# Kernel tuning notes

Measured on AMD Instinct MI355X. Metric: run time of the kernel, lower is better.

Reference implementation:

```python
import jax, jax.numpy as jnp
import numpy as np

B = 16384; NF = 16; VOCAB = 100000; ED = 32; NNUM = 13
E = 8; T = 2; H0 = 512; H1 = 256; TH = 128
D0 = NF * ED + NNUM  # 525
EPS = 1e-5


def setup_inputs() -> dict:
    key = jax.random.key(0)
    ks = jax.random.split(key, 24)
    f32 = jnp.float32
    return {
        "categorical_x": jax.random.randint(ks[0], (B, NF), 0, VOCAB),
        "numerical_x": jax.random.normal(ks[1], (B, NNUM), f32),
        "epoch": 5,  # >= M -> MoE (not if_neuron) branch
        "emb_table": jax.random.normal(ks[2], (NF * VOCAB, ED), f32) * 0.05,
        "W0": jax.random.normal(ks[3], (E, D0, H0), f32) * 0.05,
        "b0": jnp.zeros((E, H0), f32),
        "bn0_gamma": 1.0 + 0.1 * jax.random.normal(ks[4], (H0,), f32),
        "bn0_beta": 0.1 * jax.random.normal(ks[5], (H0,), f32),
        "bn0_mean": 0.1 * jax.random.normal(ks[6], (H0,), f32),
        "bn0_var": 0.5 + jax.random.uniform(ks[7], (H0,), f32),
        "W1": jax.random.normal(ks[8], (E, H0, H1), f32) * 0.05,
        "b1": jnp.zeros((E, H1), f32),
        "bn1_gamma": 1.0 + 0.1 * jax.random.normal(ks[9], (H1,), f32),
        "bn1_beta": 0.1 * jax.random.normal(ks[10], (H1,), f32),
        "bn1_mean": 0.1 * jax.random.normal(ks[11], (H1,), f32),
        "bn1_var": 0.5 + jax.random.uniform(ks[12], (H1,), f32),
        "Wg": jax.random.normal(ks[13], (T, D0, E), f32) * 0.05,
        "bg": jnp.zeros((T, E), f32),
        "Wt1": jax.random.normal(ks[14], (T, H1, TH), f32) * 0.05,
        "bt1": jnp.zeros((T, TH), f32),
        "tbn_gamma": 1.0 + 0.1 * jax.random.normal(ks[15], (T, TH), f32),
        "tbn_beta": 0.1 * jax.random.normal(ks[16], (T, TH), f32),
        "tbn_mean": 0.1 * jax.random.normal(ks[17], (T, TH), f32),
        "tbn_var": 0.5 + jax.random.uniform(ks[18], (T, TH), f32),
        "Wt2": jax.random.normal(ks[19], (T, TH, 1), f32) * 0.05,
        "bt2": jnp.zeros((T, 1), f32),
    }


def reference(categorical_x, numerical_x, epoch, emb_table,
              W0, b0, bn0_gamma, bn0_beta, bn0_mean, bn0_var,
              W1, b1, bn1_gamma, bn1_beta, bn1_mean, bn1_var,
              Wg, bg, Wt1, bt1, tbn_gamma, tbn_beta, tbn_mean, tbn_var,
              Wt2, bt2):
    # --- embedding + concat ---
    offsets = jnp.arange(NF, dtype=categorical_x.dtype) * VOCAB
    emb = emb_table[categorical_x + offsets[None, :]].reshape(B, NF * ED)
    x = jnp.concatenate([emb, numerical_x], axis=1)  # [B, D0]

    def bn(h, g, b, m, v):  # eval-mode BatchNorm1d, params shared across experts
        return (h - m) * jax.lax.rsqrt(v + EPS) * g + b

    # --- per-expert layer 0: grouped GEMM + shared BN/ReLU (Dropout eval=id) ---
    h = jnp.einsum('bd,edk->ebk', x, W0) + b0[:, None, :]          # [E,B,H0]
    h = jax.nn.relu(bn(h, bn0_gamma, bn0_beta, bn0_mean, bn0_var))
    # --- per-expert layer 1 ---
    h = jnp.einsum('ebd,edk->ebk', h, W1) + b1[:, None, :]          # [E,B,H1]
    h = jax.nn.relu(bn(h, bn1_gamma, bn1_beta, bn1_mean, bn1_var))

    expert_output = jnp.transpose(h, (1, 0, 2))                     # [B,E,H1]
    # --- per-task softmax gates over the raw input, bmm combine ---
    gates = jax.nn.softmax(jnp.einsum('bd,tde->tbe', x, Wg) + bg[:, None, :], axis=-1)  # [T,B,E]
    fea = jnp.einsum('tbe,bek->tbk', gates, expert_output)          # [T,B,H1]

    # --- per-task tower MLP: Linear -> BN -> ReLU -> Linear, sigmoid ---
    t = jnp.einsum('tbk,tkh->tbh', fea, Wt1) + bt1[:, None, :]      # [T,B,TH]
    t = (t - tbn_mean[:, None, :]) * jax.lax.rsqrt(tbn_var[:, None, :] + EPS)
    t = jax.nn.relu(t * tbn_gamma[:, None, :] + tbn_beta[:, None, :])
    out = (jnp.einsum('tbh,tho->tbo', t, Wt2) + bt2[:, None, :])[..., 0]  # [T,B]
    return jax.nn.sigmoid(out)
```

## Files before the change

### kernel.cpp

```cpp
#include <hip/hip_runtime.h>
#include <hip/hip_bf16.h>

#define B_ 16384
#define NF_ 16
#define VOCAB_ 100000
#define ED_ 32
#define NNUM_ 13
#define E_ 8
#define T_ 2
#define H0_ 512
#define H1_ 256
#define TH_ 128
#define D0_ 525
#define K0P 640

typedef __bf16 bf16x8 __attribute__((ext_vector_type(8)));
typedef float  f32x4  __attribute__((ext_vector_type(4)));

typedef __attribute__((address_space(3))) void lds_void;
typedef __attribute__((address_space(1))) const void gbl_void;

__device__ __forceinline__ void load_lds16f(const void* g, void* l) {
  __builtin_amdgcn_global_load_lds((gbl_void*)g, (lds_void*)l, 16, 0, 0);
}

#define BARX                                        \
  do {                                              \
    asm volatile("" ::: "memory");                  \
    __builtin_amdgcn_s_barrier();                   \
    __builtin_amdgcn_sched_barrier(0);              \
    asm volatile("" ::: "memory");                  \
  } while (0)
#define LGKM0                                       \
  do {                                              \
    asm volatile("s_waitcnt lgkmcnt(0)" ::: "memory"); \
    __builtin_amdgcn_sched_barrier(0);              \
  } while (0)

__global__ __launch_bounds__(256) void k_embed(const int* __restrict__ cat,
                                               const float* __restrict__ num,
                                               const float* __restrict__ emb,
                                               __hip_bfloat16* __restrict__ x) {
  int b = blockIdx.x;
  int t = threadIdx.x;
  const int* crow = cat + b * NF_;
#pragma unroll
  for (int i = 0; i < 3; ++i) {
    int d = t + i * 256;
    if (d >= K0P) continue;
    float v;
    if (d < 512) {
      int f = d >> 5, c = d & 31;
      v = emb[((long long)(f * VOCAB_ + crow[f])) * ED_ + c];
    } else if (d < D0_) {
      v = num[b * NNUM_ + (d - 512)];
    } else {
      v = 0.f;
    }
    x[(long long)b * K0P + d] = __float2bfloat16(v);
  }
}

__global__ __launch_bounds__(256) void k_wprep(const float* __restrict__ W,
                                               __hip_bfloat16* __restrict__ Wp,
                                               int K, int N, int KP) {
  __shared__ float tile[64][65];
  int k0 = blockIdx.x * 64, n0 = blockIdx.y * 64, e = blockIdx.z;
  int tx = threadIdx.x & 63, ty = threadIdx.x >> 6;
  for (int r = ty; r < 64; r += 4) {
    int k = k0 + r;
    tile[r][tx] = (k < K) ? W[((long long)e * K + k) * N + n0 + tx] : 0.f;
  }
  __syncthreads();
  for (int r = ty; r < 64; r += 4) {
    int n = n0 + r;
    Wp[((long long)e * N + n) * KP + k0 + tx] = __float2bfloat16(tile[tx][r]);
  }
}

__global__ void k_prep_small(const float* b0, const float* g0, const float* be0,
                             const float* m0, const float* v0,
                             const float* b1, const float* g1, const float* be1,
                             const float* m1, const float* v1,
                             const float* bt1, const float* tg, const float* tb,
                             const float* tm, const float* tv,
                             float* scale0, float* ebias0, float* scale1, float* ebias1,
                             float* tscale, float* tbias) {
  int i = blockIdx.x * 256 + threadIdx.x;
  if (i < H0_) scale0[i] = g0[i] * rsqrtf(v0[i] + 1e-5f);
  if (i < H1_) scale1[i] = g1[i] * rsqrtf(v1[i] + 1e-5f);
  if (i < T_ * TH_) {
    float s = tg[i] * rsqrtf(tv[i] + 1e-5f);
    tscale[i] = s;
    tbias[i] = (bt1[i] - tm[i]) * s + tb[i];
  }
  if (i < E_ * H0_) {
    int n = i & (H0_ - 1);
    float s = g0[n] * rsqrtf(v0[n] + 1e-5f);
    ebias0[i] = (b0[i] - m0[n]) * s + be0[n];
  }
  if (i < E_ * H1_) {
    int n = i & (H1_ - 1);
    float s = g1[n] * rsqrtf(v1[n] + 1e-5f);
    ebias1[i] = (b1[i] - m1[n]) * s + be1[n];
  }
}

__global__ __launch_bounds__(256) void k_gates(const __hip_bfloat16* __restrict__ x,
                                               const float* __restrict__ Wg,
                                               const float* __restrict__ bg,
                                               float* __restrict__ gates) {
  int gidx = blockIdx.x * 256 + threadIdx.x;
  int b = gidx >> 4, te = gidx & 15;
  int t = te >> 3, e = te & 7;
  const __hip_bfloat16* xr = x + (long long)b * K0P;
  const float* wg = Wg + ((long long)t * D0_) * E_ + e;
  float acc = bg[t * E_ + e];
  int k = 0;
  for (; k + 8 <= D0_; k += 8) {
    bf16x8 xv = *reinterpret_cast<const bf16x8*>(xr + k);
#pragma unroll
    for (int j = 0; j < 8; ++j)
      acc += (float)xv[j] * wg[(long long)(k + j) * E_];
  }
  for (; k < D0_; ++k) acc += __bfloat162float(xr[k]) * wg[(long long)k * E_];
  float mx = acc;
#pragma unroll
  for (int o = 1; o < 8; o <<= 1) mx = fmaxf(mx, __shfl_xor(mx, o));
  float p = __expf(acc - mx);
  float s = p;
#pragma unroll
  for (int o = 1; o < 8; o <<= 1) s += __shfl_xor(s, o);
  gates[((long long)t * B_ + b) * E_ + e] = p / s;
}

__global__ __launch_bounds__(512, 2) void k_gemm(
    const __hip_bfloat16* __restrict__ Aall, long long strideAe, int lda,
    const __hip_bfloat16* __restrict__ Ball, long long strideBe, int ldb,
    __hip_bfloat16* __restrict__ Call, long long strideCe, int N,
    const float* __restrict__ scale, const float* __restrict__ ebias, int strideEb,
    int K) {
  __shared__ __align__(16) char As[2][2][16384];
  __shared__ __align__(16) char Bs[2][2][16384];

  const int e = blockIdx.z;
  const char* A = reinterpret_cast<const char*>(Aall + (long long)e * strideAe +
                                                (long long)blockIdx.x * 256 * lda);
  const char* Bw = reinterpret_cast<const char*>(Ball + (long long)e * strideBe +
                                                 (long long)blockIdx.y * 256 * ldb);
  const int ldab = lda * 2, ldbb = ldb * 2;

  const int tid = threadIdx.x;
  const int lane = tid & 63;
  const int wid = tid >> 6;
  const int wq_r = wid >> 2, wq_c = wid & 3;

  const int srow = tid >> 3;
  const int swz = ((tid & 7) << 4) ^ ((srow & 7) << 4);

  auto STG_A = [&](int kt, int half, int slot) {
#pragma unroll
    for (int j = 0; j < 2; ++j) {
      const int lrow = srow + j * 64;
      load_lds16f(A + (long long)(half * 128 + lrow) * ldab + kt * 128 + swz,
                  &As[slot][half][j * 8192 + tid * 16]);
    }
  };
  auto STG_B = [&](int kt, int half, int slot) {
#pragma unroll
    for (int j = 0; j < 2; ++j) {
      const int lrow = srow + j * 64;
      load_lds16f(Bw + (long long)(half * 128 + lrow) * ldbb + kt * 128 + swz,
                  &Bs[slot][half][j * 8192 + tid * 16]);
    }
  };

  bf16x8 af[2][4], bq[2][2];
  auto LDA = [&](int slot, int half) {
#pragma unroll
    for (int kk = 0; kk < 2; ++kk) {
      const int kb = kk * 64 + (lane >> 4) * 16;
#pragma unroll
      for (int m = 0; m < 4; ++m) {
        const int lrow = wq_r * 64 + m * 16 + (lane & 15);
        af[kk][m] = *reinterpret_cast<const bf16x8*>(
            &As[slot][half][lrow * 128 + (kb ^ ((lane & 7) << 4))]);
      }
    }
  };
  auto LDB = [&](int slot, int half) {
#pragma unroll
    for (int kk = 0; kk < 2; ++kk) {
      const int kb = kk * 64 + (lane >> 4) * 16;
#pragma unroll
      for (int n = 0; n < 2; ++n) {
        const int lrow = wq_c * 32 + n * 16 + (lane & 15);
        bq[kk][n] = *reinterpret_cast<const bf16x8*>(
            &Bs[slot][half][lrow * 128 + (kb ^ ((lane & 7) << 4))]);
      }
    }
  };

  f32x4 acc[2][2][4][2];
#pragma unroll
  for (int a = 0; a < 2; ++a)
#pragma unroll
    for (int b = 0; b < 2; ++b)
#pragma unroll
      for (int m = 0; m < 4; ++m)
#pragma unroll
        for (int n = 0; n < 2; ++n) acc[a][b][m][n] = (f32x4){0.f, 0.f, 0.f, 0.f};

#define MMQ(QM, QN)                                                            \
  do {                                                                         \
    __builtin_amdgcn_s_setprio(1);                                             \
    _Pragma("unroll") for (int kk = 0; kk < 2; ++kk)                           \
        _Pragma("unroll") for (int m = 0; m < 4; ++m)                          \
            _Pragma("unroll") for (int n = 0; n < 2; ++n)                      \
                acc[QM][QN][m][n] = __builtin_amdgcn_mfma_f32_16x16x32_bf16(   \
                    af[kk][m], bq[kk][n], acc[QM][QN][m][n], 0, 0, 0);         \
    __builtin_amdgcn_s_setprio(0);                                             \
  } while (0)

  const int nk = K / 64;
  const int nj = nk / 2;

  STG_A(0, 0, 0); STG_A(0, 1, 0); STG_B(0, 0, 0); STG_B(0, 1, 0);
  if (nk > 1) { STG_A(1, 0, 1); STG_B(1, 1, 1); }
  asm volatile("s_waitcnt vmcnt(4)" ::: "memory");
  BARX;

  for (int j = 0; j < nj; ++j) {
    const int t1 = 2 * j + 1, t2 = 2 * j + 2, t3 = 2 * j + 3;
    const bool more = (t2 < nk);
    LDA(0, 0); LDB(0, 0);
    STG_A(t1, 1, 1);
    BARX; LGKM0; MMQ(0, 0); BARX;
    LDB(0, 1);
    STG_B(t1, 0, 1);
    BARX; LGKM0; MMQ(0, 1); BARX;
    LDA(0, 1);
    if (more) STG_A(t2, 0, 0);
    BARX; LGKM0; MMQ(1, 1); BARX;
    LDB(0, 0);
    if (more) STG_B(t2, 1, 0);
    BARX; LGKM0; MMQ(1, 0);
    if (more) { asm volatile("s_waitcnt vmcnt(4)" ::: "memory"); }
    else      { asm volatile("s_waitcnt vmcnt(0)" ::: "memory"); }
    BARX;
    LDA(1, 0); LDB(1, 0);
    if (more) STG_A(t2, 1, 0);
    BARX; LGKM0; MMQ(0, 0); BARX;
    LDB(1, 1);
    if (more) STG_B(t2, 0, 0);
    BARX; LGKM0; MMQ(0, 1); BARX;
    LDA(1, 1);
    if (more) STG_A(t3, 0, 1);
    BARX; LGKM0; MMQ(1, 1); BARX;
    LDB(1, 0);
    if (more) STG_B(t3, 1, 1);
    BARX; LGKM0; MMQ(1, 0);
    if (more) { asm volatile("s_waitcnt vmcnt(4)" ::: "memory"); }
    BARX;
  }
#undef MMQ

  __hip_bfloat16* C = Call + (long long)e * strideCe;
  const float* eb = ebias + e * strideEb;
  const int m0 = blockIdx.x * 256, n0 = blockIdx.y * 256;
#pragma unroll
  for (int Qm = 0; Qm < 2; ++Qm)
#pragma unroll
    for (int Qn = 0; Qn < 2; ++Qn)
#pragma unroll
      for (int n = 0; n < 2; ++n) {
        const int col = n0 + Qn * 128 + wq_c * 32 + n * 16 + (lane & 15);
        const float s = scale[col];
        const float bb = eb[col];
#pragma unroll
        for (int m = 0; m < 4; ++m) {
          const int rowb = m0 + Qm * 128 + wq_r * 64 + m * 16 + (lane >> 4) * 4;
#pragma unroll
          for (int i = 0; i < 4; ++i) {
            float v = fmaxf(acc[Qm][Qn][m][n][i] * s + bb, 0.f);
            C[(long long)(rowb + i) * N + col] = __float2bfloat16(v);
          }
        }
      }
}

__global__ __launch_bounds__(256) void k_combine(const __hip_bfloat16* __restrict__ h1,
                                                 const float* __restrict__ gates,
                                                 __hip_bfloat16* __restrict__ fea) {
  const int idx = blockIdx.x * 256 + threadIdx.x;
  const int b = idx >> 5, c = idx & 31;
  const f32x4* gp0 = reinterpret_cast<const f32x4*>(gates + (long long)b * E_);
  const f32x4* gp1 = reinterpret_cast<const f32x4*>(gates + ((long long)B_ + b) * E_);
  const f32x4 g0lo = gp0[0], g0hi = gp0[1];
  const f32x4 g1lo = gp1[0], g1hi = gp1[1];

  float a0[8], a1[8];
#pragma unroll
  for (int j = 0; j < 8; ++j) { a0[j] = 0.f; a1[j] = 0.f; }

#pragma unroll
  for (int ee = 0; ee < 8; ++ee) {
    bf16x8 hv = *reinterpret_cast<const bf16x8*>(
        h1 + ((long long)ee * B_ + b) * H1_ + c * 8);
    const float ga = (ee < 4) ? g0lo[ee & 3] : g0hi[ee & 3];
    const float gb = (ee < 4) ? g1lo[ee & 3] : g1hi[ee & 3];
#pragma unroll
    for (int j = 0; j < 8; ++j) {
      float v = (float)hv[j];
      a0[j] += ga * v;
      a1[j] += gb * v;
    }
  }
  bf16x8 o0, o1;
#pragma unroll
  for (int j = 0; j < 8; ++j) { o0[j] = (__bf16)a0[j]; o1[j] = (__bf16)a1[j]; }
  *reinterpret_cast<bf16x8*>(fea + (long long)b * H1_ + c * 8) = o0;
  *reinterpret_cast<bf16x8*>(fea + ((long long)B_ + b) * H1_ + c * 8) = o1;
}

__global__ __launch_bounds__(256) void k_tower2(
    const __hip_bfloat16* __restrict__ fea, const float* __restrict__ Wt1,
    const float* __restrict__ Wt2, const float* __restrict__ bt2,
    const float* __restrict__ tscale, const float* __restrict__ tbias,
    float* __restrict__ out) {
  __shared__ __align__(16) char Ws[TH_ * 512];
  const int t = blockIdx.y;
  const int tid = threadIdx.x;
  const int lane = tid & 63, wv = tid >> 6;

  const int row = blockIdx.x * 64 + wv * 16 + (lane & 15);
  const int g4 = lane >> 4;

  for (int it = 0; it < 16; ++it) {
    int idx = it * 256 + tid;
    int h = idx & 127, kc = idx >> 7;
    bf16x8 v;
#pragma unroll
    for (int j = 0; j < 8; ++j)
      v[j] = (__bf16)Wt1[((long long)t * H1_ + kc * 8 + j) * TH_ + h];
    int byt = h * 512 + ((kc * 16) ^ ((h & 7) << 4));
    *reinterpret_cast<bf16x8*>(Ws + byt) = v;
  }

  bf16x8 af[8];
  {
    const __hip_bfloat16* fp = fea + ((long long)t * B_ + row) * H1_ + g4 * 8;
#pragma unroll
    for (int c = 0; c < 8; ++c)
      af[c] = *reinterpret_cast<const bf16x8*>(fp + c * 32);
  }
  __syncthreads();

  f32x4 acc[8];
#pragma unroll
  for (int n = 0; n < 8; ++n) acc[n] = (f32x4){0.f, 0.f, 0.f, 0.f};
#pragma unroll
  for (int c = 0; c < 8; ++c) {
    int kb = c * 64 + g4 * 16;
#pragma unroll
    for (int n = 0; n < 8; ++n) {
      int hrow = n * 16 + (lane & 15);
      bf16x8 bv = *reinterpret_cast<const bf16x8*>(Ws + hrow * 512 + (kb ^ ((hrow & 7) << 4)));
      acc[n] = __builtin_amdgcn_mfma_f32_16x16x32_bf16(af[c], bv, acc[n], 0, 0, 0);
    }
  }

  float part[4] = {0.f, 0.f, 0.f, 0.f};
#pragma unroll
  for (int n = 0; n < 8; ++n) {
    int col = n * 16 + (lane & 15);
    float s = tscale[t * TH_ + col], bb = tbias[t * TH_ + col], w2 = Wt2[t * TH_ + col];
#pragma unroll
    for (int i = 0; i < 4; ++i)
      part[i] += fmaxf(acc[n][i] * s + bb, 0.f) * w2;
  }
#pragma unroll
  for (int o = 1; o < 16; o <<= 1) {
#pragma unroll
    for (int i = 0; i < 4; ++i) part[i] += __shfl_xor(part[i], o);
  }
  if ((lane & 15) == 0) {
    int rbase = blockIdx.x * 64 + wv * 16 + g4 * 4;
    float b2 = bt2[t];
#pragma unroll
    for (int i = 0; i < 4; ++i) {
      float z = part[i] + b2;
      out[(long long)t * B_ + rbase + i] = 1.f / (1.f + __expf(-z));
    }
  }
}

extern "C" void kernel_launch(void* const* d_in, const int* in_sizes, int n_in,
                              void* d_out, int out_size, void* d_ws, size_t ws_size,
                              hipStream_t stream) {
  const int*   cat = (const int*)d_in[0];
  const float* num = (const float*)d_in[1];
  const float* emb = (const float*)d_in[3];
  const float* W0  = (const float*)d_in[4];
  const float* b0  = (const float*)d_in[5];
  const float* g0  = (const float*)d_in[6];
  const float* be0 = (const float*)d_in[7];
  const float* m0  = (const float*)d_in[8];
  const float* v0  = (const float*)d_in[9];
  const float* W1  = (const float*)d_in[10];
  const float* b1  = (const float*)d_in[11];
  const float* g1  = (const float*)d_in[12];
  const float* be1 = (const float*)d_in[13];
  const float* m1  = (const float*)d_in[14];
  const float* v1  = (const float*)d_in[15];
  const float* Wg  = (const float*)d_in[16];
  const float* bg  = (const float*)d_in[17];
  const float* Wt1 = (const float*)d_in[18];
  const float* bt1 = (const float*)d_in[19];
  const float* tg  = (const float*)d_in[20];
  const float* tb  = (const float*)d_in[21];
  const float* tm  = (const float*)d_in[22];
  const float* tv  = (const float*)d_in[23];
  const float* Wt2 = (const float*)d_in[24];
  const float* bt2 = (const float*)d_in[25];
  float* out = (float*)d_out;

  char* ws = (char*)d_ws;
  if (ws_size < 247496704ULL) return;

  __hip_bfloat16* x_bf = (__hip_bfloat16*)(ws + 0ULL);
  __hip_bfloat16* W0p  = (__hip_bfloat16*)(ws + 20971520ULL);
  __hip_bfloat16* W1p  = (__hip_bfloat16*)(ws + 26214400ULL);
  float* gates   = (float*)(ws + 28311552ULL);
  float* scale0  = (float*)(ws + 29360128ULL);
  float* ebias0  = (float*)(ws + 29362176ULL);
  float* scale1  = (float*)(ws + 29378560ULL);
  float* ebias1  = (float*)(ws + 29379584ULL);
  float* tscale  = (float*)(ws + 29387776ULL);
  float* tbias   = (float*)(ws + 29388800ULL);
  __hip_bfloat16* h0  = (__hip_bfloat16*)(ws + 29392896ULL);
  __hip_bfloat16* h1  = (__hip_bfloat16*)(ws + 163610624ULL);
  __hip_bfloat16* fea = (__hip_bfloat16*)(ws + 230719488ULL);

  k_wprep<<<dim3(K0P / 64, H0_ / 64, E_), 256, 0, stream>>>(W0, W0p, D0_, H0_, K0P);
  k_wprep<<<dim3(H0_ / 64, H1_ / 64, E_), 256, 0, stream>>>(W1, W1p, H0_, H1_, H0_);
  k_prep_small<<<16, 256, 0, stream>>>(b0, g0, be0, m0, v0, b1, g1, be1, m1, v1,
                                       bt1, tg, tb, tm, tv,
                                       scale0, ebias0, scale1, ebias1, tscale, tbias);
  k_embed<<<B_, 256, 0, stream>>>(cat, num, emb, x_bf);
  k_gates<<<B_ * 16 / 256, 256, 0, stream>>>(x_bf, Wg, bg, gates);
  k_gemm<<<dim3(B_ / 256, H0_ / 256, E_), 512, 0, stream>>>(
      x_bf, 0LL, K0P, W0p, (long long)H0_ * K0P, K0P,
      h0, (long long)B_ * H0_, H0_, scale0, ebias0, H0_, K0P);
  k_gemm<<<dim3(B_ / 256, H1_ / 256, E_), 512, 0, stream>>>(
      h0, (long long)B_ * H0_, H0_, W1p, (long long)H1_ * H0_, H0_,
      h1, (long long)B_ * H1_, H1_, scale1, ebias1, H1_, H0_);
  k_combine<<<B_ * H1_ / 8 / 256, 256, 0, stream>>>(h1, gates, fea);
  k_tower2<<<dim3(B_ / 64, T_), 256, 0, stream>>>(fea, Wt1, Wt2, bt2,
                                                  tscale, tbias, out);
}
```

Baseline: 257.6 us.

## Trim layer-0 K padding and stage GEMM epilogue through LDS for coalesced stores

Reduces the padded K of the first expert GEMM from 640 to 576, which gives an odd number of 64-wide K tiles. To support that, the main loop gets a separate guard for the third prefetch and a tail step that handles the final odd tile. The epilogue now writes bf16 results into swizzled shared memory (reusing the staging buffers) and then stores 16-byte rows to global memory, replacing scattered 2-byte stores. This removes wasted MFMA work on padding and uncoalesced output writes, at the cost of an extra barrier and a shared-memory round trip.

```diff
diff --git a/kernel.cpp b/kernel.cpp
--- a/kernel.cpp
+++ b/kernel.cpp
@@ -12,7 +12,7 @@
 #define H1_ 256
 #define TH_ 128
 #define D0_ 525
-#define K0P 640
+#define K0P 576
 
 typedef __bf16 bf16x8 __attribute__((ext_vector_type(8)));
 typedef float  f32x4  __attribute__((ext_vector_type(4)));
@@ -140,8 +140,9 @@
     __hip_bfloat16* __restrict__ Call, long long strideCe, int N,
     const float* __restrict__ scale, const float* __restrict__ ebias, int strideEb,
     int K) {
-  __shared__ __align__(16) char As[2][2][16384];
-  __shared__ __align__(16) char Bs[2][2][16384];
+  __shared__ __align__(16) char SMEM[131072];
+  char (*As)[2][16384] = reinterpret_cast<char (*)[2][16384]>(SMEM);
+  char (*Bs)[2][16384] = reinterpret_cast<char (*)[2][16384]>(SMEM + 65536);
 
   const int e = blockIdx.z;
   const char* A = reinterpret_cast<const char*>(Aall + (long long)e * strideAe +
@@ -223,7 +224,7 @@
   } while (0)
 
   const int nk = K / 64;
-  const int nj = nk / 2;
+  const int nj = nk >> 1;
 
   STG_A(0, 0, 0); STG_A(0, 1, 0); STG_B(0, 0, 0); STG_B(0, 1, 0);
   if (nk > 1) { STG_A(1, 0, 1); STG_B(1, 1, 1); }
@@ -233,6 +234,7 @@
   for (int j = 0; j < nj; ++j) {
     const int t1 = 2 * j + 1, t2 = 2 * j + 2, t3 = 2 * j + 3;
     const bool more = (t2 < nk);
+    const bool more3 = (t3 < nk);
     LDA(0, 0); LDB(0, 0);
     STG_A(t1, 1, 1);
     BARX; LGKM0; MMQ(0, 0); BARX;
@@ -255,16 +257,26 @@
     if (more) STG_B(t2, 0, 0);
     BARX; LGKM0; MMQ(0, 1); BARX;
     LDA(1, 1);
-    if (more) STG_A(t3, 0, 1);
+    if (more3) STG_A(t3, 0, 1);
     BARX; LGKM0; MMQ(1, 1); BARX;
     LDB(1, 0);
-    if (more) STG_B(t3, 1, 1);
+    if (more3) STG_B(t3, 1, 1);
     BARX; LGKM0; MMQ(1, 0);
     if (more) { asm volatile("s_waitcnt vmcnt(4)" ::: "memory"); }
     BARX;
   }
+
+  if (nk & 1) {
+    asm volatile("s_waitcnt vmcnt(0)" ::: "memory");
+    BARX;
+    LDA(0, 0); LDB(0, 0); LGKM0; MMQ(0, 0);
+    LDB(0, 1);            LGKM0; MMQ(0, 1);
+    LDA(0, 1);            LGKM0; MMQ(1, 1);
+    LDB(0, 0);            LGKM0; MMQ(1, 0);
+  }
 #undef MMQ
 
+  __syncthreads();
   __hip_bfloat16* C = Call + (long long)e * strideCe;
   const float* eb = ebias + e * strideEb;
   const int m0 = blockIdx.x * 256, n0 = blockIdx.y * 256;
@@ -274,19 +286,30 @@
     for (int Qn = 0; Qn < 2; ++Qn)
 #pragma unroll
       for (int n = 0; n < 2; ++n) {
-        const int col = n0 + Qn * 128 + wq_c * 32 + n * 16 + (lane & 15);
-        const float s = scale[col];
-        const float bb = eb[col];
+        const int col = Qn * 128 + wq_c * 32 + n * 16 + (lane & 15);
+        const float s = scale[n0 + col];
+        const float bb = eb[n0 + col];
 #pragma unroll
         for (int m = 0; m < 4; ++m) {
-          const int rowb = m0 + Qm * 128 + wq_r * 64 + m * 16 + (lane >> 4) * 4;
 #pragma unroll
           for (int i = 0; i < 4; ++i) {
-            float v = fmaxf(acc[Qm][Qn][m][n][i] * s + bb, 0.f);
-            C[(long long)(rowb + i) * N + col] = __float2bfloat16(v);
+            const int row = Qm * 128 + wq_r * 64 + m * 16 + (lane >> 4) * 4 + i;
+            const float v = fmaxf(acc[Qm][Qn][m][n][i] * s + bb, 0.f);
+            const int byt = row * 512 + ((((col >> 3) ^ (row & 7)) << 4) | ((col & 7) << 1));
+            *reinterpret_cast<__hip_bfloat16*>(SMEM + byt) = __float2bfloat16(v);
           }
         }
       }
+  __syncthreads();
+#pragma unroll
+  for (int it = 0; it < 16; ++it) {
+    const int row = it * 16 + (tid >> 5);
+    const int c16 = tid & 31;
+    const f32x4 d = *reinterpret_cast<const f32x4*>(
+        SMEM + row * 512 + ((c16 ^ (row & 7)) << 4));
+    *reinterpret_cast<f32x4*>(
+        reinterpret_cast<char*>(C + (long long)(m0 + row) * N + n0) + c16 * 16) = d;
+  }
 }
 
 __global__ __launch_bounds__(256) void k_combine(const __hip_bfloat16* __restrict__ h1,
```

After: 402.8 us. 1.56x slower.

## Make grouped GEMMs persistent with cross-tile prefetch and LDS-staged coalesced epilogue

Applied to the files above, without the earlier changes.

Replaces the per-tile GEMM grid with a persistent kernel of 256 blocks. Each block walks several consecutive output tiles (4 for layer 0, 2 for layer 1), and the k-loop pipeline runs continuously across tile boundaries, so the next tile's loads overlap the current tile's tail. The epilogue now writes through a swizzled LDS buffer so global stores are 16-byte coalesced instead of scattered 2-byte writes, and tile order is remapped across blocks. The costs are one block per CU (launch bounds drop from 2 to 1), a 160KB LDS footprint, and extra barriers inside the epilogue.

```diff
diff --git a/kernel.cpp b/kernel.cpp
--- a/kernel.cpp
+++ b/kernel.cpp
@@ -134,21 +134,22 @@
   gates[((long long)t * B_ + b) * E_ + e] = p / s;
 }
 
-__global__ __launch_bounds__(512, 2) void k_gemm(
-    const __hip_bfloat16* __restrict__ Aall, long long strideAe, int lda,
-    const __hip_bfloat16* __restrict__ Ball, long long strideBe, int ldb,
-    __hip_bfloat16* __restrict__ Call, long long strideCe, int N,
-    const float* __restrict__ scale, const float* __restrict__ ebias, int strideEb,
-    int K) {
-  __shared__ __align__(16) char As[2][2][16384];
-  __shared__ __align__(16) char Bs[2][2][16384];
-
-  const int e = blockIdx.z;
-  const char* A = reinterpret_cast<const char*>(Aall + (long long)e * strideAe +
-                                                (long long)blockIdx.x * 256 * lda);
-  const char* Bw = reinterpret_cast<const char*>(Ball + (long long)e * strideBe +
-                                                 (long long)blockIdx.y * 256 * ldb);
-  const int ldab = lda * 2, ldbb = ldb * 2;
+template <int KC, int NNY, int TPB>
+__global__ __launch_bounds__(512, 1) void k_gemmp(
+    const __hip_bfloat16* __restrict__ Aall, long long strideAe,
+    const __hip_bfloat16* __restrict__ Ball, long long strideBe,
+    __hip_bfloat16* __restrict__ Call, long long strideCe,
+    const float* __restrict__ scale, const float* __restrict__ ebias,
+    int strideEb) {
+  constexpr int NK = KC / 64;
+  constexpr int S = TPB * NK;
+  constexpr int P = S / 2;
+  constexpr int PPT = NK / 2;
+  constexpr int N = NNY * 256;
+  constexpr int LDAB = KC * 2;
+
+  __shared__ __align__(16) char SMEM[163840];
+  char* const Ebuf = SMEM + 131072;
 
   const int tid = threadIdx.x;
   const int lane = tid & 63;
@@ -158,25 +159,42 @@
   const int srow = tid >> 3;
   const int swz = ((tid & 7) << 4) ^ ((srow & 7) << 4);
 
-  auto STG_A = [&](int kt, int half, int slot) {
+  const int c = blockIdx.x;
+  const int vbase = ((c & 7) * 32 + (c >> 3)) * TPB;
+
+  auto decode = [&](int v, int& mx, int& ny, int& e) {
+    mx = v & 63;
+    int p = v >> 6;
+    if (NNY == 2) { ny = p & 1; e = p >> 1; }
+    else          { ny = 0;     e = p;      }
+  };
+
+  auto STG = [&](int s, int half, bool isB) {
+    const int ot = s / NK, kt = s - ot * NK;
+    int mx, ny, e;
+    decode(vbase + ot, mx, ny, e);
+    const char* base;
+    char* dst;
+    if (!isB) {
+      base = reinterpret_cast<const char*>(Aall + (long long)e * strideAe +
+                                           (long long)mx * 256 * KC);
+      dst = SMEM + (s & 1) * 32768 + half * 16384;
+    } else {
+      base = reinterpret_cast<const char*>(Ball + (long long)e * strideBe +
+                                           (long long)ny * 256 * KC);
+      dst = SMEM + 65536 + (s & 1) * 32768 + half * 16384;
+    }
 #pragma unroll
     for (int j = 0; j < 2; ++j) {
       const int lrow = srow + j * 64;
-      load_lds16f(A + (long long)(half * 128 + lrow) * ldab + kt * 128 + swz,
-                  &As[slot][half][j * 8192 + tid * 16]);
-    }
-  };
-  auto STG_B = [&](int kt, int half, int slot) {
-#pragma unroll
-    for (int j = 0; j < 2; ++j) {
-      const int lrow = srow + j * 64;
-      load_lds16f(Bw + (long long)(half * 128 + lrow) * ldbb + kt * 128 + swz,
-                  &Bs[slot][half][j * 8192 + tid * 16]);
+      load_lds16f(base + (long long)(half * 128 + lrow) * LDAB + kt * 128 + swz,
+                  dst + j * 8192 + tid * 16);
     }
   };
 
   bf16x8 af[2][4], bq[2][2];
   auto LDA = [&](int slot, int half) {
+    const char* Ab = SMEM + slot * 32768 + half * 16384;
 #pragma unroll
     for (int kk = 0; kk < 2; ++kk) {
       const int kb = kk * 64 + (lane >> 4) * 16;
@@ -184,11 +202,12 @@
       for (int m = 0; m < 4; ++m) {
         const int lrow = wq_r * 64 + m * 16 + (lane & 15);
         af[kk][m] = *reinterpret_cast<const bf16x8*>(
-            &As[slot][half][lrow * 128 + (kb ^ ((lane & 7) << 4))]);
+            Ab + lrow * 128 + (kb ^ ((lane & 7) << 4)));
       }
     }
   };
   auto LDB = [&](int slot, int half) {
+    const char* Bb = SMEM + 65536 + slot * 32768 + half * 16384;
 #pragma unroll
     for (int kk = 0; kk < 2; ++kk) {
       const int kb = kk * 64 + (lane >> 4) * 16;
@@ -196,7 +215,7 @@
       for (int n = 0; n < 2; ++n) {
         const int lrow = wq_c * 32 + n * 16 + (lane & 15);
         bq[kk][n] = *reinterpret_cast<const bf16x8*>(
-            &Bs[slot][half][lrow * 128 + (kb ^ ((lane & 7) << 4))]);
+            Bb + lrow * 128 + (kb ^ ((lane & 7) << 4)));
       }
     }
   };
@@ -222,71 +241,99 @@
     __builtin_amdgcn_s_setprio(0);                                             \
   } while (0)
 
-  const int nk = K / 64;
-  const int nj = nk / 2;
-
-  STG_A(0, 0, 0); STG_A(0, 1, 0); STG_B(0, 0, 0); STG_B(0, 1, 0);
-  if (nk > 1) { STG_A(1, 0, 1); STG_B(1, 1, 1); }
+  STG(0, 0, false); STG(0, 1, false); STG(0, 0, true); STG(0, 1, true);
+  STG(1, 0, false); STG(1, 1, true);
   asm volatile("s_waitcnt vmcnt(4)" ::: "memory");
   BARX;
 
-  for (int j = 0; j < nj; ++j) {
-    const int t1 = 2 * j + 1, t2 = 2 * j + 2, t3 = 2 * j + 3;
-    const bool more = (t2 < nk);
+  int ot_done = 0;
+#pragma unroll 1
+  for (int p = 0; p < P; ++p) {
+    const int t1 = 2 * p + 1, t2 = 2 * p + 2, t3 = 2 * p + 3;
+    const bool m2 = (t2 < S), m3 = (t3 < S);
     LDA(0, 0); LDB(0, 0);
-    STG_A(t1, 1, 1);
+    STG(t1, 1, false);
     BARX; LGKM0; MMQ(0, 0); BARX;
     LDB(0, 1);
-    STG_B(t1, 0, 1);
+    STG(t1, 0, true);
     BARX; LGKM0; MMQ(0, 1); BARX;
     LDA(0, 1);
-    if (more) STG_A(t2, 0, 0);
+    if (m2) STG(t2, 0, false);
     BARX; LGKM0; MMQ(1, 1); BARX;
     LDB(0, 0);
-    if (more) STG_B(t2, 1, 0);
+    if (m2) STG(t2, 1, true);
     BARX; LGKM0; MMQ(1, 0);
-    if (more) { asm volatile("s_waitcnt vmcnt(4)" ::: "memory"); }
-    else      { asm volatile("s_waitcnt vmcnt(0)" ::: "memory"); }
+    if (m2) { asm volatile("s_waitcnt vmcnt(4)" ::: "memory"); }
+    else    { asm volatile("s_waitcnt vmcnt(0)" ::: "memory"); }
     BARX;
     LDA(1, 0); LDB(1, 0);
-    if (more) STG_A(t2, 1, 0);
+    if (m2) STG(t2, 1, false);
     BARX; LGKM0; MMQ(0, 0); BARX;
     LDB(1, 1);
-    if (more) STG_B(t2, 0, 0);
+    if (m2) STG(t2, 0, true);
     BARX; LGKM0; MMQ(0, 1); BARX;
     LDA(1, 1);
-    if (more) STG_A(t3, 0, 1);
+    if (m3) STG(t3, 0, false);
     BARX; LGKM0; MMQ(1, 1); BARX;
     LDB(1, 0);
-    if (more) STG_B(t3, 1, 1);
+    if (m3) STG(t3, 1, true);
     BARX; LGKM0; MMQ(1, 0);
-    if (more) { asm volatile("s_waitcnt vmcnt(4)" ::: "memory"); }
+    if (m2) { asm volatile("s_waitcnt vmcnt(4)" ::: "memory"); }
     BARX;
+
+    if ((p + 1) % PPT == 0) {
+      int mx, ny, e;
+      decode(vbase + ot_done, mx, ny, e);
+      __hip_bfloat16* C = Call + (long long)e * strideCe;
+      const float* eb = ebias + e * strideEb;
+      const int m0 = mx * 256, n0 = ny * 256;
+#pragma unroll
+      for (int Qm = 0; Qm < 2; ++Qm)
+#pragma unroll
+        for (int Qn = 0; Qn < 2; ++Qn) {
+#pragma unroll
+          for (int n = 0; n < 2; ++n) {
+            const int colc = wq_c * 32 + n * 16 + (lane & 15);
+            const int gcol = n0 + Qn * 128 + colc;
+            const float s = scale[gcol];
+            const float bb = eb[gcol];
+#pragma unroll
+            for (int m = 0; m < 4; ++m) {
+#pragma unroll
+              for (int i = 0; i < 4; ++i) {
+                const int row = wq_r * 64 + m * 16 + (lane >> 4) * 4 + i;
+                const float v = fmaxf(acc[Qm][Qn][m][n][i] * s + bb, 0.f);
+                const int byt = row * 256 +
+                    ((((colc >> 3) ^ (row & 7)) << 4) | ((colc & 7) << 1));
+                *reinterpret_cast<__hip_bfloat16*>(Ebuf + byt) = __float2bfloat16(v);
+              }
+            }
+          }
+          BARX;
+#pragma unroll
+          for (int it = 0; it < 4; ++it) {
+            const int r = it * 32 + (tid >> 4);
+            const int c16 = tid & 15;
+            const f32x4 d = *reinterpret_cast<const f32x4*>(
+                Ebuf + r * 256 + ((c16 ^ (r & 7)) << 4));
+            *reinterpret_cast<f32x4*>(
+                reinterpret_cast<char*>(C + (long long)(m0 + Qm * 128 + r) * N) +
+                (n0 + Qn * 128) * 2 + c16 * 16) = d;
+          }
+          BARX;
+        }
+      ++ot_done;
+#pragma unroll
+      for (int a = 0; a < 2; ++a)
+#pragma unroll
+        for (int b = 0; b < 2; ++b)
+#pragma unroll
+          for (int m = 0; m < 4; ++m)
+#pragma unroll
+            for (int n = 0; n < 2; ++n) acc[a][b][m][n] = (f32x4){0.f, 0.f, 0.f, 0.f};
+    }
   }
 #undef MMQ
-
-  __hip_bfloat16* C = Call + (long long)e * strideCe;
-  const float* eb = ebias + e * strideEb;
-  const int m0 = blockIdx.x * 256, n0 = blockIdx.y * 256;
-#pragma unroll
-  for (int Qm = 0; Qm < 2; ++Qm)
-#pragma unroll
-    for (int Qn = 0; Qn < 2; ++Qn)
-#pragma unroll
-      for (int n = 0; n < 2; ++n) {
-        const int col = n0 + Qn * 128 + wq_c * 32 + n * 16 + (lane & 15);
-        const float s = scale[col];
-        const float bb = eb[col];
-#pragma unroll
-        for (int m = 0; m < 4; ++m) {
-          const int rowb = m0 + Qm * 128 + wq_r * 64 + m * 16 + (lane >> 4) * 4;
-#pragma unroll
-          for (int i = 0; i < 4; ++i) {
-            float v = fmaxf(acc[Qm][Qn][m][n][i] * s + bb, 0.f);
-            C[(long long)(rowb + i) * N + col] = __float2bfloat16(v);
-          }
-        }
-      }
 }
 
 __global__ __launch_bounds__(256) void k_combine(const __hip_bfloat16* __restrict__ h1,
@@ -449,12 +496,12 @@
                                        scale0, ebias0, scale1, ebias1, tscale, tbias);
   k_embed<<<B_, 256, 0, stream>>>(cat, num, emb, x_bf);
   k_gates<<<B_ * 16 / 256, 256, 0, stream>>>(x_bf, Wg, bg, gates);
-  k_gemm<<<dim3(B_ / 256, H0_ / 256, E_), 512, 0, stream>>>(
-      x_bf, 0LL, K0P, W0p, (long long)H0_ * K0P, K0P,
-      h0, (long long)B_ * H0_, H0_, scale0, ebias0, H0_, K0P);
-  k_gemm<<<dim3(B_ / 256, H1_ / 256, E_), 512, 0, stream>>>(
-      h0, (long long)B_ * H0_, H0_, W1p, (long long)H1_ * H0_, H0_,
-      h1, (long long)B_ * H1_, H1_, scale1, ebias1, H1_, H0_);
+  k_gemmp<K0P, 2, 4><<<256, 512, 0, stream>>>(
+      x_bf, 0LL, W0p, (long long)H0_ * K0P,
+      h0, (long long)B_ * H0_, scale0, ebias0, H0_);
+  k_gemmp<H0_, 1, 2><<<256, 512, 0, stream>>>(
+      h0, (long long)B_ * H0_, W1p, (long long)H1_ * H0_,
+      h1, (long long)B_ * H1_, scale1, ebias1, H1_);
   k_combine<<<B_ * H1_ / 8 / 256, 256, 0, stream>>>(h1, gates, fea);
   k_tower2<<<dim3(B_ / 64, T_), 256, 0, stream>>>(fea, Wt1, Wt2, bt2,
                                                   tscale, tbias, out);
```

Measured after the change: 270.6 us. +5.0%, slower.
